# Performance work log

Hardware: AMD Instinct MI355X
Metric: run time of the kernel (lower is better)

The kernel has to match this reference:

```python
import jax, jax.numpy as jnp
import numpy as np
from jax import lax

ALPHA = 2.0  # ATan surrogate alpha (spikingjelly default)
V_TH = 1.0   # threshold; v_reset = 0.0 (hard reset)

@jax.custom_vjp
def spike_fn(x):
    return (x >= 0.0).astype(x.dtype)

def _spike_fwd(x):
    return spike_fn(x), x

def _spike_bwd(x, g):
    # ATan surrogate: alpha/2 / (1 + (pi/2*alpha*x)^2)
    sg = (ALPHA / 2.0) / (1.0 + (jnp.pi / 2.0 * ALPHA * x) ** 2)
    return (g * sg,)

spike_fn.defvjp(_spike_fwd, _spike_bwd)

def conv_bn(x_seq, w, gamma, beta, mean, var, eps=1e-5):
    # x_seq: [T,B,C,H,W]; conv+BN applied over flattened T*B (SeqToANNContainer)
    T, B, C, H, W = x_seq.shape
    y = lax.conv_general_dilated(
        x_seq.reshape(T * B, C, H, W), w,
        window_strides=(1, 1), padding='SAME',
        dimension_numbers=('NCHW', 'OIHW', 'NCHW'))
    inv = gamma / jnp.sqrt(var + eps)
    y = y * inv[None, :, None, None] + (beta - mean * inv)[None, :, None, None]
    Co = w.shape[0]
    return y.reshape(T, B, Co, H, W)

def plif(x_seq, w):
    # Parametric LIF: v <- v + (x - v) * sigmoid(w); hard reset to 0; detach_reset
    k = jax.nn.sigmoid(w)
    def step(v, x):
        v = v + (x - v) * k
        s = spike_fn(v - V_TH)
        v = v * (1.0 - lax.stop_gradient(s))
        return v, s
    _, s_seq = lax.scan(step, jnp.zeros_like(x_seq[0]), x_seq)
    return s_seq

def setup_inputs() -> dict:
    key = jax.random.key(0)
    ks = jax.random.split(key, 4)
    T, B, C, H, W = 4, 8, 128, 56, 56
    mid = 128
    x = (jax.random.uniform(ks[0], (T, B, C, H, W), jnp.float32) < 0.5).astype(jnp.float32)
    conv1_w = jax.random.normal(ks[1], (mid, C, 3, 3), jnp.float32) * (1.0 / np.sqrt(C * 9))
    conv2_w = jax.random.normal(ks[2], (C, mid, 3, 3), jnp.float32) * (1.0 / np.sqrt(mid * 9))
    return {
        'x': x,
        'conv1_w': conv1_w,
        'gamma1': jnp.ones((mid,), jnp.float32), 'beta1': jnp.zeros((mid,), jnp.float32),
        'mean1': jnp.zeros((mid,), jnp.float32), 'var1': jnp.ones((mid,), jnp.float32),
        'w1': jnp.float32(0.0),  # init_tau=2.0 -> w = -log(tau-1) = 0
        'conv2_w': conv2_w,
        'gamma2': jnp.ones((C,), jnp.float32), 'beta2': jnp.zeros((C,), jnp.float32),
        'mean2': jnp.zeros((C,), jnp.float32), 'var2': jnp.ones((C,), jnp.float32),
        'w2': jnp.float32(0.0),
    }

def reference(x, conv1_w, gamma1, beta1, mean1, var1, w1,
              conv2_w, gamma2, beta2, mean2, var2, w2):
    s1 = plif(conv_bn(x, conv1_w, gamma1, beta1, mean1, var1), w1)
    s2 = plif(conv_bn(s1, conv2_w, gamma2, beta2, mean2, var2), w2)
    out = s2 + x  # connect_f == 'ADD'
    return out
```

## Files before the change

kernel.cpp:

```cpp
#include <hip/hip_runtime.h>
#include <math.h>

#define T_ 4
#define B_ 8
#define C_ 128
#define H_ 56
#define W_ 56
#define NIMG (T_ * B_)
#define HW (H_ * W_)
#define NLOC ((size_t)B_ * C_ * HW)
#define NE ((size_t)T_ * NLOC)

typedef __attribute__((ext_vector_type(4))) int   int4v;
typedef __attribute__((ext_vector_type(4))) float float4v;

#define GLOAD_LDS16(gp, lp) \
    __builtin_amdgcn_global_load_lds((const __attribute__((address_space(1))) unsigned int*)(gp), \
                                     (__attribute__((address_space(3))) unsigned int*)(lp), 16, 0, 0)

__global__ __launch_bounds__(128) void scale_k(const float* __restrict__ w,
                                               float* __restrict__ sv) {
    __shared__ float red[128];
    int co = blockIdx.x, t = threadIdx.x;
    const float* p = w + (size_t)co * 1152 + t * 9;
    float m = 0.f;
#pragma unroll
    for (int j = 0; j < 9; ++j) m = fmaxf(m, fabsf(p[j]));
    red[t] = m; __syncthreads();
    for (int off = 64; off; off >>= 1) {
        if (t < off) red[t] = fmaxf(red[t], red[t + off]);
        __syncthreads();
    }
    if (t == 0) sv[co] = fmaxf(red[0], 1e-20f) / 127.f;
}

__global__ __launch_bounds__(256) void repack_k(const float* __restrict__ w,
                                                const float* __restrict__ sv,
                                                signed char* __restrict__ Bs) {
    int idx = blockIdx.x * 256 + threadIdx.x;
    if (idx >= 9 * 1024) return;
    int tap = idx >> 10;
    int rem = idx & 1023;
    int co = rem >> 3, cig = rem & 7;
    double s = (double)sv[co];
    union { signed char b[16]; int4v v; } q[3];
#pragma unroll
    for (int e = 0; e < 16; ++e) {
        int ci = cig * 16 + e;
        double v = (double)w[((size_t)co * 128 + ci) * 9 + tap];
        double q1 = rint(v / s);
        double r1 = v - s * q1;
        double q2 = rint(r1 * 128.0 / s);
        double r2 = r1 - s * q2 * 0.0078125;
        double q3 = rint(r2 * 16384.0 / s);
        q[0].b[e] = (signed char)(int)q1;
        q[1].b[e] = (signed char)(int)q2;
        q[2].b[e] = (signed char)(int)q3;
    }
    int Lb = co * 128 + ((cig ^ (co & 7)) << 4);
#pragma unroll
    for (int sp = 0; sp < 3; ++sp)
        *(int4v*)(Bs + (size_t)(tap * 3 + sp) * 16384 + Lb) = q[sp].v;
}

__global__ __launch_bounds__(256) void xpose_k(const float* __restrict__ x,
                                               signed char* __restrict__ Xt) {
    __shared__ float xs[128][57];
    int n = blockIdx.x / 56, h = blockIdx.x % 56;
    int tid = threadIdx.x;
    const float* xp = x + (size_t)n * 128 * HW + h * 56;
#pragma unroll
    for (int j = 0; j < 7; ++j) {
        int idx = tid + j * 256;
        int c = idx / 14, wq = idx - c * 14;
        float4 v = *(const float4*)(xp + (size_t)c * HW + wq * 4);
        xs[c][wq * 4 + 0] = v.x; xs[c][wq * 4 + 1] = v.y;
        xs[c][wq * 4 + 2] = v.z; xs[c][wq * 4 + 3] = v.w;
    }
    __syncthreads();
    signed char* Op = Xt + ((size_t)n * HW + h * 56) * 128;
#pragma unroll
    for (int j = 0; j < 2; ++j) {
        int idx = tid + j * 256;
        if (idx < 448) {
            int ww = idx >> 3, sl = idx & 7;
            int cg = sl ^ (ww & 7);
            union { signed char b[16]; int4v v; } u;
#pragma unroll
            for (int e = 0; e < 16; ++e)
                u.b[e] = (xs[cg * 16 + e][ww] >= 0.5f) ? 1 : 0;
            *(int4v*)(Op + ww * 128 + sl * 16) = u.v;
        }
    }
}

__global__ __launch_bounds__(512, 2) void conv_mfma_k(
        const signed char* __restrict__ Xt,
        const signed char* __restrict__ Bs,
        const float* __restrict__ sv,
        const float* __restrict__ gamma, const float* __restrict__ beta,
        const float* __restrict__ mean,  const float* __restrict__ var,
        float* __restrict__ Y) {
    __shared__ signed char aA[4 * 8192];
    __shared__ signed char bB[3 * 16384];

    const int tid = threadIdx.x;
    const int lane = tid & 63;
    const int wave = tid >> 6;
    const int fr = lane & 15, fq = lane >> 4;
    const int row_local = wave >> 2;
    const int q = wave & 3;
    const int img = blockIdx.x / 28;
    const int h0 = (blockIdx.x % 28) * 2;
    const int h = h0 + row_local;

#define STAGE3(tp) do {                                                           \
        const char* _src = (const char*)Bs + (size_t)(tp) * 49152 + tid * 16;     \
        char* _dst = (char*)bB + tid * 16;                                        \
        _Pragma("unroll")                                                         \
        for (int _c = 0; _c < 6; ++_c)                                            \
            GLOAD_LDS16(_src + _c * 8192, _dst + _c * 8192);                      \
    } while (0)

#define LOADA(tp) do {                                                            \
        int _dh = (tp) / 3, _dw = (tp) - ((tp) / 3) * 3;                          \
        int _hh = h + _dh - 1;                                                    \
        bool _hok = (unsigned)_hh < 56u;                                          \
        int _r4 = row_local + _dh;                                                \
        _Pragma("unroll")                                                         \
        for (int _m = 0; _m < 4; ++_m) {                                          \
            int _px = _m * 16 + fr + _dw - 1;                                     \
            bool _ok = _hok && ((unsigned)_px < 56u);                             \
            int _pxc = _ok ? _px : 0;                                             \
            const signed char* _base = aA + _r4 * 8192 + _pxc * 128;              \
            _Pragma("unroll")                                                     \
            for (int _ks = 0; _ks < 2; ++_ks) {                                   \
                int _sl = (_ks * 4 + fq) ^ (_pxc & 7);                            \
                int4v _v = *(const int4v*)(_base + _sl * 16);                     \
                a[_m][_ks] = _ok ? _v : zi;                                       \
            }                                                                     \
        }                                                                         \
    } while (0)

    const int tap0 = (int)((blockIdx.x * 4u) % 9u);

    {
        const signed char* XtN = Xt + (size_t)img * HW * 128;
#pragma unroll
        for (int i = 0; i < 4; ++i) {
            int hh = h0 - 1 + i;
            hh = hh < 0 ? 0 : (hh > 55 ? 55 : hh);
            const char* src = (const char*)(XtN + (size_t)hh * 7168);
            GLOAD_LDS16(src + tid * 16, (char*)aA + i * 8192 + tid * 16);
        }
        STAGE3(tap0);
        asm volatile("s_waitcnt vmcnt(0)" ::: "memory");
        __builtin_amdgcn_sched_barrier(0);
        __builtin_amdgcn_s_barrier();
    }

    const int4v zi = (int4v){0, 0, 0, 0};
    int4v acc[3][4][2];
#pragma unroll
    for (int sp = 0; sp < 3; ++sp)
#pragma unroll
        for (int m = 0; m < 4; ++m) {
            acc[sp][m][0] = zi; acc[sp][m][1] = zi;
        }
    int4v a[4][2];
    LOADA(tap0);

    const int cob = (q * 32 + fr) * 128;
    const int sl0 = (fq ^ (fr & 7)) << 4;
    const int sl1 = ((4 + fq) ^ (fr & 7)) << 4;

    for (int it = 0; it < 9; ++it) {
        int tap = tap0 + it; if (tap >= 9) tap -= 9;

        __builtin_amdgcn_s_setprio(1);
#pragma unroll
        for (int sp = 0; sp < 3; ++sp) {
            const signed char* bp = bB + sp * 16384;
            int4v b00 = *(const int4v*)(bp + cob + sl0);
            int4v b10 = *(const int4v*)(bp + cob + sl1);
            int4v b01 = *(const int4v*)(bp + cob + 2048 + sl0);
            int4v b11 = *(const int4v*)(bp + cob + 2048 + sl1);
#pragma unroll
            for (int m = 0; m < 4; ++m) {
                acc[sp][m][0] = __builtin_amdgcn_mfma_i32_16x16x64_i8(a[m][0], b00, acc[sp][m][0], 0, 0, 0);
                acc[sp][m][0] = __builtin_amdgcn_mfma_i32_16x16x64_i8(a[m][1], b10, acc[sp][m][0], 0, 0, 0);
                acc[sp][m][1] = __builtin_amdgcn_mfma_i32_16x16x64_i8(a[m][0], b01, acc[sp][m][1], 0, 0, 0);
                acc[sp][m][1] = __builtin_amdgcn_mfma_i32_16x16x64_i8(a[m][1], b11, acc[sp][m][1], 0, 0, 0);
            }
        }
        __builtin_amdgcn_s_setprio(0);
        __builtin_amdgcn_s_barrier();

        if (it < 8) {
            int ntap = tap + 1; if (ntap >= 9) ntap -= 9;
            STAGE3(ntap);
            LOADA(ntap);
            asm volatile("s_waitcnt vmcnt(0)" ::: "memory");
            __builtin_amdgcn_sched_barrier(0);
            __builtin_amdgcn_s_barrier();
        }
    }

    float* Yp = Y + ((size_t)img * HW + h * 56) * 128;
#pragma unroll
    for (int nf = 0; nf < 2; ++nf) {
        int co = q * 32 + nf * 16 + fr;
        float s = sv[co];
        float iv = gamma[co] / sqrtf(var[co] + 1e-5f);
        float mul = s * iv;
        float bs = beta[co] - mean[co] * iv;
#pragma unroll
        for (int m = 0; m < 4; ++m)
#pragma unroll
            for (int r = 0; r < 4; ++r) {
                int ww = m * 16 + fq * 4 + r;
                if (ww < 56) {
                    float val = (float)acc[0][m][nf][r]
                              + (float)acc[1][m][nf][r] * 0.0078125f
                              + (float)acc[2][m][nf][r] * 6.103515625e-05f;
                    Yp[(size_t)ww * 128 + co] = fmaf(val, mul, bs);
                }
            }
    }
#undef STAGE3
#undef LOADA
}

__global__ __launch_bounds__(256) void plif1_k(const float* __restrict__ Y,
                                               const float* __restrict__ wp,
                                               signed char* __restrict__ S) {
    int gid = blockIdx.x * 256 + threadIdx.x;
    int cg = gid & 7;
    int pix = gid >> 3;
    int w = (pix % HW) % 56;
    float k = 1.f / (1.f + expf(-wp[0]));
    float v[16];
#pragma unroll
    for (int e = 0; e < 16; ++e) v[e] = 0.f;
    size_t base = (size_t)pix * 128 + cg * 16;
    size_t obase = (size_t)pix * 128 + ((cg ^ (w & 7)) << 4);
#pragma unroll
    for (int t = 0; t < 4; ++t) {
        const float* yp = Y + (size_t)t * NLOC + base;
        union { signed char b[16]; int4v iv; } u;
#pragma unroll
        for (int e4 = 0; e4 < 4; ++e4) {
            float4 xv = *(const float4*)(yp + e4 * 4);
            float xe[4] = {xv.x, xv.y, xv.z, xv.w};
#pragma unroll
            for (int j = 0; j < 4; ++j) {
                int e = e4 * 4 + j;
                v[e] = v[e] + (xe[j] - v[e]) * k;
                bool sp = v[e] >= 1.f;
                u.b[e] = sp ? 1 : 0;
                v[e] = sp ? 0.f : v[e];
            }
        }
        *(int4v*)(S + (size_t)t * NLOC + obase) = u.iv;
    }
}

__global__ __launch_bounds__(256) void plif2_k(const float* __restrict__ Y2,
                                               const float* __restrict__ wp,
                                               const float* __restrict__ x,
                                               float* __restrict__ out) {
    __shared__ float xs[4 * 56 * 65];
    int bid = blockIdx.x;
    int half = bid & 1;
    int bh = bid >> 1;
    int b = bh / 56, h = bh % 56;
    int tid = threadIdx.x;
    float k = 1.f / (1.f + expf(-wp[0]));
#pragma unroll
    for (int j = 0; j < 14; ++j) {
        int idx = tid + j * 256;
        int t = idx / 896;
        int rem = idx - t * 896;
        int ww = rem >> 4, cq = rem & 15;
        float4 v = *(const float4*)(Y2 + ((size_t)(t * 8 + b) * HW + h * 56 + ww) * 128
                                       + half * 64 + cq * 4);
        float* dst = &xs[(t * 56 + ww) * 65 + cq * 4];
        dst[0] = v.x; dst[1] = v.y; dst[2] = v.z; dst[3] = v.w;
    }
    __syncthreads();
#pragma unroll
    for (int j = 0; j < 14; ++j) {
        int idx = tid + j * 256;
        int c = idx / 56, ww = idx - c * 56;
        float v = 0.f;
        size_t xo = ((size_t)b * 128 + half * 64 + c) * HW + h * 56 + ww;
#pragma unroll
        for (int t = 0; t < 4; ++t) {
            float yv = xs[(t * 56 + ww) * 65 + c];
            v = v + (yv - v) * k;
            bool sp = v >= 1.f;
            size_t o = xo + (size_t)t * NLOC;
            out[o] = (sp ? 1.f : 0.f) + x[o];
            v = sp ? 0.f : v;
        }
    }
}

extern "C" void kernel_launch(void* const* d_in, const int* in_sizes, int n_in,
                              void* d_out, int out_size, void* d_ws, size_t ws_size,
                              hipStream_t stream) {
    const float* x    = (const float*)d_in[0];
    const float* w1   = (const float*)d_in[1];
    const float* g1   = (const float*)d_in[2];
    const float* be1  = (const float*)d_in[3];
    const float* mu1  = (const float*)d_in[4];
    const float* va1  = (const float*)d_in[5];
    const float* tau1 = (const float*)d_in[6];
    const float* w2   = (const float*)d_in[7];
    const float* g2   = (const float*)d_in[8];
    const float* be2  = (const float*)d_in[9];
    const float* mu2  = (const float*)d_in[10];
    const float* va2  = (const float*)d_in[11];
    const float* tau2 = (const float*)d_in[12];
    float* out = (float*)d_out;

    char* ws = (char*)d_ws;
    signed char* bufA = (signed char*)ws;
    float* bufY = (float*)(ws + NE);
    float* sv1  = (float*)(ws + 5 * NE);
    float* sv2  = sv1 + 128;
    signed char* Bs1 = (signed char*)(ws + 5 * NE + 1024);
    signed char* Bs2 = Bs1 + 27 * 16384;

    scale_k<<<128, 128, 0, stream>>>(w1, sv1);
    scale_k<<<128, 128, 0, stream>>>(w2, sv2);
    repack_k<<<36, 256, 0, stream>>>(w1, sv1, Bs1);
    repack_k<<<36, 256, 0, stream>>>(w2, sv2, Bs2);
    xpose_k<<<NIMG * 56, 256, 0, stream>>>(x, bufA);

    conv_mfma_k<<<NIMG * 28, 512, 0, stream>>>(bufA, Bs1, sv1, g1, be1, mu1, va1, bufY);
    plif1_k<<<784, 256, 0, stream>>>(bufY, tau1, bufA);
    conv_mfma_k<<<NIMG * 28, 512, 0, stream>>>(bufA, Bs2, sv2, g2, be2, mu2, va2, bufY);
    plif2_k<<<B_ * 56 * 2, 256, 0, stream>>>(bufY, tau2, x, out);
}
```

Measured before the change: 197.8 us.

## Fuse conv with PLIF over time steps and double-buffer weight staging

Each conv block now loops over all four time steps of a batch image instead of handling one image. It keeps the PLIF membrane state in registers and applies BN, the spike update and either the int8 spike store or the residual add directly in the epilogue. This removes the fp32 intermediate write/read and the two separate PLIF kernels, and weight taps are double-buffered in LDS with partial vmcnt waits to overlap loads with MFMA. The trade-off is a grid cut to 224 large blocks with higher LDS use, which lowers occupancy and leaves some CUs idle.

```diff
diff --git a/kernel.cpp b/kernel.cpp
--- a/kernel.cpp
+++ b/kernel.cpp
@@ -12,7 +12,6 @@
 #define NE ((size_t)T_ * NLOC)
 
 typedef __attribute__((ext_vector_type(4))) int   int4v;
-typedef __attribute__((ext_vector_type(4))) float float4v;
 
 #define GLOAD_LDS16(gp, lp) \
     __builtin_amdgcn_global_load_lds((const __attribute__((address_space(1))) unsigned int*)(gp), \
@@ -94,15 +93,19 @@
     }
 }
 
-__global__ __launch_bounds__(512, 2) void conv_mfma_k(
-        const signed char* __restrict__ Xt,
+template<int MODE>
+__global__ __launch_bounds__(512) void convplif_k(
+        const signed char* __restrict__ Xin,
         const signed char* __restrict__ Bs,
         const float* __restrict__ sv,
         const float* __restrict__ gamma, const float* __restrict__ beta,
         const float* __restrict__ mean,  const float* __restrict__ var,
-        float* __restrict__ Y) {
+        const float* __restrict__ tau,
+        const float* __restrict__ xres,
+        void* __restrict__ outp) {
     __shared__ signed char aA[4 * 8192];
-    __shared__ signed char bB[3 * 16384];
+    __shared__ signed char bB[2][49152];
+    __shared__ signed char sS[2 * 8192];
 
     const int tid = threadIdx.x;
     const int lane = tid & 63;
@@ -110,13 +113,35 @@
     const int fr = lane & 15, fq = lane >> 4;
     const int row_local = wave >> 2;
     const int q = wave & 3;
-    const int img = blockIdx.x / 28;
+    const int bb = blockIdx.x / 28;
     const int h0 = (blockIdx.x % 28) * 2;
     const int h = h0 + row_local;
-
-#define STAGE3(tp) do {                                                           \
+    const int tap0 = (int)((blockIdx.x * 4u) % 9u);
+
+    const float kk = 1.f / (1.f + expf(-tau[0]));
+    float mulv[2], bsv[2];
+#pragma unroll
+    for (int nf = 0; nf < 2; ++nf) {
+        int co = q * 32 + nf * 16 + fr;
+        float iv = gamma[co] / sqrtf(var[co] + 1e-5f);
+        mulv[nf] = sv[co] * iv;
+        bsv[nf] = beta[co] - mean[co] * iv;
+    }
+
+#define STAGEA(tt) do {                                                           \
+        const signed char* _XtN = Xin + (size_t)((tt) * 8 + bb) * (HW * 128);     \
+        _Pragma("unroll")                                                         \
+        for (int _i = 0; _i < 4; ++_i) {                                          \
+            int _hh = h0 - 1 + _i;                                                \
+            _hh = _hh < 0 ? 0 : (_hh > 55 ? 55 : _hh);                            \
+            GLOAD_LDS16((const char*)(_XtN + (size_t)_hh * 7168) + tid * 16,      \
+                        (char*)aA + _i * 8192 + tid * 16);                        \
+        }                                                                         \
+    } while (0)
+
+#define STAGEB(tp, buf) do {                                                      \
         const char* _src = (const char*)Bs + (size_t)(tp) * 49152 + tid * 16;     \
-        char* _dst = (char*)bB + tid * 16;                                        \
+        char* _dst = (char*)&bB[(buf)][0] + tid * 16;                             \
         _Pragma("unroll")                                                         \
         for (int _c = 0; _c < 6; ++_c)                                            \
             GLOAD_LDS16(_src + _c * 8192, _dst + _c * 8192);                      \
@@ -142,31 +167,25 @@
         }                                                                         \
     } while (0)
 
-    const int tap0 = (int)((blockIdx.x * 4u) % 9u);
-
-    {
-        const signed char* XtN = Xt + (size_t)img * HW * 128;
-#pragma unroll
-        for (int i = 0; i < 4; ++i) {
-            int hh = h0 - 1 + i;
-            hh = hh < 0 ? 0 : (hh > 55 ? 55 : hh);
-            const char* src = (const char*)(XtN + (size_t)hh * 7168);
-            GLOAD_LDS16(src + tid * 16, (char*)aA + i * 8192 + tid * 16);
-        }
-        STAGE3(tap0);
-        asm volatile("s_waitcnt vmcnt(0)" ::: "memory");
-        __builtin_amdgcn_sched_barrier(0);
-        __builtin_amdgcn_s_barrier();
-    }
+    STAGEA(0);
+    STAGEB(tap0, 0);
+    asm volatile("s_waitcnt vmcnt(0)" ::: "memory");
+    __builtin_amdgcn_sched_barrier(0);
+    __builtin_amdgcn_s_barrier();
 
     const int4v zi = (int4v){0, 0, 0, 0};
     int4v acc[3][4][2];
 #pragma unroll
     for (int sp = 0; sp < 3; ++sp)
 #pragma unroll
-        for (int m = 0; m < 4; ++m) {
-            acc[sp][m][0] = zi; acc[sp][m][1] = zi;
-        }
+        for (int m = 0; m < 4; ++m) { acc[sp][m][0] = zi; acc[sp][m][1] = zi; }
+    float v[2][4][4];
+#pragma unroll
+    for (int nf = 0; nf < 2; ++nf)
+#pragma unroll
+        for (int m = 0; m < 4; ++m)
+#pragma unroll
+            for (int r = 0; r < 4; ++r) v[nf][m][r] = 0.f;
     int4v a[4][2];
     LOADA(tap0);
 
@@ -174,13 +193,25 @@
     const int sl0 = (fq ^ (fr & 7)) << 4;
     const int sl1 = ((4 + fq) ^ (fr & 7)) << 4;
 
-    for (int it = 0; it < 9; ++it) {
-        int tap = tap0 + it; if (tap >= 9) tap -= 9;
-
+    int tap = tap0, it = 0, t = 0;
+    for (int g = 0; g < 36; ++g) {
+        const int ntap = (tap + 1 == 9) ? 0 : tap + 1;
+        const bool tend = (it == 8);
+        if (tend && t < 3) STAGEA(t + 1);
+        if (g < 35) {
+            STAGEB(ntap, (g + 1) & 1);
+            asm volatile("s_waitcnt vmcnt(6)" ::: "memory");
+        } else {
+            asm volatile("s_waitcnt vmcnt(0)" ::: "memory");
+        }
+        __builtin_amdgcn_sched_barrier(0);
+        __builtin_amdgcn_s_barrier();
+
+        const signed char* bbase = &bB[g & 1][0];
         __builtin_amdgcn_s_setprio(1);
 #pragma unroll
         for (int sp = 0; sp < 3; ++sp) {
-            const signed char* bp = bB + sp * 16384;
+            const signed char* bp = bbase + sp * 16384;
             int4v b00 = *(const int4v*)(bp + cob + sl0);
             int4v b10 = *(const int4v*)(bp + cob + sl1);
             int4v b01 = *(const int4v*)(bp + cob + 2048 + sl0);
@@ -194,116 +225,90 @@
             }
         }
         __builtin_amdgcn_s_setprio(0);
+
+        if (g < 35) LOADA(ntap);
+        asm volatile("s_waitcnt lgkmcnt(0)" ::: "memory");
+        __builtin_amdgcn_sched_barrier(0);
         __builtin_amdgcn_s_barrier();
 
-        if (it < 8) {
-            int ntap = tap + 1; if (ntap >= 9) ntap -= 9;
-            STAGE3(ntap);
-            LOADA(ntap);
-            asm volatile("s_waitcnt vmcnt(0)" ::: "memory");
-            __builtin_amdgcn_sched_barrier(0);
-            __builtin_amdgcn_s_barrier();
-        }
-    }
-
-    float* Yp = Y + ((size_t)img * HW + h * 56) * 128;
-#pragma unroll
-    for (int nf = 0; nf < 2; ++nf) {
-        int co = q * 32 + nf * 16 + fr;
-        float s = sv[co];
-        float iv = gamma[co] / sqrtf(var[co] + 1e-5f);
-        float mul = s * iv;
-        float bs = beta[co] - mean[co] * iv;
-#pragma unroll
-        for (int m = 0; m < 4; ++m)
-#pragma unroll
-            for (int r = 0; r < 4; ++r) {
-                int ww = m * 16 + fq * 4 + r;
-                if (ww < 56) {
-                    float val = (float)acc[0][m][nf][r]
-                              + (float)acc[1][m][nf][r] * 0.0078125f
-                              + (float)acc[2][m][nf][r] * 6.103515625e-05f;
-                    Yp[(size_t)ww * 128 + co] = fmaf(val, mul, bs);
+        if (tend) {
+            if (MODE == 0) {
+                signed char* S1 = (signed char*)outp;
+#pragma unroll
+                for (int nf = 0; nf < 2; ++nf)
+#pragma unroll
+                    for (int m = 0; m < 4; ++m)
+#pragma unroll
+                        for (int r = 0; r < 4; ++r) {
+                            int px = m * 16 + fq * 4 + r;
+                            float val = (float)acc[0][m][nf][r]
+                                      + (float)acc[1][m][nf][r] * 0.0078125f
+                                      + (float)acc[2][m][nf][r] * 6.103515625e-05f;
+                            float y = fmaf(val, mulv[nf], bsv[nf]);
+                            float vv = v[nf][m][r];
+                            vv = vv + (y - vv) * kk;
+                            bool spk = vv >= 1.f;
+                            v[nf][m][r] = spk ? 0.f : vv;
+                            sS[row_local * 8192 + px * 128 + q * 32 + nf * 16 + fr] = spk ? 1 : 0;
+                        }
+                asm volatile("s_waitcnt lgkmcnt(0)" ::: "memory");
+                __builtin_amdgcn_s_barrier();
+                const size_t imgb = (size_t)(t * 8 + bb) * HW;
+#pragma unroll
+                for (int cc = 0; cc < 2; ++cc) {
+                    int chunk = tid + cc * 512;
+                    int row = chunk >> 9, rem = chunk & 511;
+                    int px = rem >> 3, cg = rem & 7;
+                    if (px < 56) {
+                        int4v v16 = *(const int4v*)(sS + row * 8192 + px * 128 + cg * 16);
+                        *(int4v*)(S1 + (imgb + (size_t)(h0 + row) * 56 + px) * 128
+                                     + ((cg ^ (px & 7)) << 4)) = v16;
+                    }
+                }
+            } else {
+                float* outw = (float*)outp;
+#pragma unroll
+                for (int nf = 0; nf < 2; ++nf) {
+                    const size_t cobase = ((size_t)(t * 8 + bb) * 128 + q * 32 + nf * 16 + fr) * HW
+                                        + (size_t)h * 56;
+#pragma unroll
+                    for (int m = 0; m < 4; ++m) {
+                        int px0 = m * 16 + fq * 4;
+                        float o4[4];
+#pragma unroll
+                        for (int r = 0; r < 4; ++r) {
+                            float val = (float)acc[0][m][nf][r]
+                                      + (float)acc[1][m][nf][r] * 0.0078125f
+                                      + (float)acc[2][m][nf][r] * 6.103515625e-05f;
+                            float y = fmaf(val, mulv[nf], bsv[nf]);
+                            float vv = v[nf][m][r];
+                            vv = vv + (y - vv) * kk;
+                            bool spk = vv >= 1.f;
+                            v[nf][m][r] = spk ? 0.f : vv;
+                            o4[r] = spk ? 1.f : 0.f;
+                        }
+                        if (px0 < 56) {
+                            float4 xv = *(const float4*)(xres + cobase + px0);
+                            float4 ov = make_float4(o4[0] + xv.x, o4[1] + xv.y,
+                                                    o4[2] + xv.z, o4[3] + xv.w);
+                            *(float4*)(outw + cobase + px0) = ov;
+                        }
+                    }
                 }
             }
-    }
-#undef STAGE3
+#pragma unroll
+            for (int sp = 0; sp < 3; ++sp)
+#pragma unroll
+                for (int m = 0; m < 4; ++m) { acc[sp][m][0] = zi; acc[sp][m][1] = zi; }
+            t++; it = 0;
+        } else {
+            it++;
+        }
+        tap = ntap;
+    }
+#undef STAGEA
+#undef STAGEB
 #undef LOADA
-}
-
-__global__ __launch_bounds__(256) void plif1_k(const float* __restrict__ Y,
-                                               const float* __restrict__ wp,
-                                               signed char* __restrict__ S) {
-    int gid = blockIdx.x * 256 + threadIdx.x;
-    int cg = gid & 7;
-    int pix = gid >> 3;
-    int w = (pix % HW) % 56;
-    float k = 1.f / (1.f + expf(-wp[0]));
-    float v[16];
-#pragma unroll
-    for (int e = 0; e < 16; ++e) v[e] = 0.f;
-    size_t base = (size_t)pix * 128 + cg * 16;
-    size_t obase = (size_t)pix * 128 + ((cg ^ (w & 7)) << 4);
-#pragma unroll
-    for (int t = 0; t < 4; ++t) {
-        const float* yp = Y + (size_t)t * NLOC + base;
-        union { signed char b[16]; int4v iv; } u;
-#pragma unroll
-        for (int e4 = 0; e4 < 4; ++e4) {
-            float4 xv = *(const float4*)(yp + e4 * 4);
-            float xe[4] = {xv.x, xv.y, xv.z, xv.w};
-#pragma unroll
-            for (int j = 0; j < 4; ++j) {
-                int e = e4 * 4 + j;
-                v[e] = v[e] + (xe[j] - v[e]) * k;
-                bool sp = v[e] >= 1.f;
-                u.b[e] = sp ? 1 : 0;
-                v[e] = sp ? 0.f : v[e];
-            }
-        }
-        *(int4v*)(S + (size_t)t * NLOC + obase) = u.iv;
-    }
-}
-
-__global__ __launch_bounds__(256) void plif2_k(const float* __restrict__ Y2,
-                                               const float* __restrict__ wp,
-                                               const float* __restrict__ x,
-                                               float* __restrict__ out) {
-    __shared__ float xs[4 * 56 * 65];
-    int bid = blockIdx.x;
-    int half = bid & 1;
-    int bh = bid >> 1;
-    int b = bh / 56, h = bh % 56;
-    int tid = threadIdx.x;
-    float k = 1.f / (1.f + expf(-wp[0]));
-#pragma unroll
-    for (int j = 0; j < 14; ++j) {
-        int idx = tid + j * 256;
-        int t = idx / 896;
-        int rem = idx - t * 896;
-        int ww = rem >> 4, cq = rem & 15;
-        float4 v = *(const float4*)(Y2 + ((size_t)(t * 8 + b) * HW + h * 56 + ww) * 128
-                                       + half * 64 + cq * 4);
-        float* dst = &xs[(t * 56 + ww) * 65 + cq * 4];
-        dst[0] = v.x; dst[1] = v.y; dst[2] = v.z; dst[3] = v.w;
-    }
-    __syncthreads();
-#pragma unroll
-    for (int j = 0; j < 14; ++j) {
-        int idx = tid + j * 256;
-        int c = idx / 56, ww = idx - c * 56;
-        float v = 0.f;
-        size_t xo = ((size_t)b * 128 + half * 64 + c) * HW + h * 56 + ww;
-#pragma unroll
-        for (int t = 0; t < 4; ++t) {
-            float yv = xs[(t * 56 + ww) * 65 + c];
-            v = v + (yv - v) * k;
-            bool sp = v >= 1.f;
-            size_t o = xo + (size_t)t * NLOC;
-            out[o] = (sp ? 1.f : 0.f) + x[o];
-            v = sp ? 0.f : v;
-        }
-    }
 }
 
 extern "C" void kernel_launch(void* const* d_in, const int* in_sizes, int n_in,
@@ -325,21 +330,21 @@
     float* out = (float*)d_out;
 
     char* ws = (char*)d_ws;
-    signed char* bufA = (signed char*)ws;
-    float* bufY = (float*)(ws + NE);
-    float* sv1  = (float*)(ws + 5 * NE);
+    signed char* Xt  = (signed char*)ws;
+    signed char* S1  = (signed char*)(ws + NE);
+    float* sv1  = (float*)(ws + 2 * NE);
     float* sv2  = sv1 + 128;
-    signed char* Bs1 = (signed char*)(ws + 5 * NE + 1024);
+    signed char* Bs1 = (signed char*)(ws + 2 * NE + 1024);
     signed char* Bs2 = Bs1 + 27 * 16384;
 
     scale_k<<<128, 128, 0, stream>>>(w1, sv1);
     scale_k<<<128, 128, 0, stream>>>(w2, sv2);
     repack_k<<<36, 256, 0, stream>>>(w1, sv1, Bs1);
     repack_k<<<36, 256, 0, stream>>>(w2, sv2, Bs2);
-    xpose_k<<<NIMG * 56, 256, 0, stream>>>(x, bufA);
-
-    conv_mfma_k<<<NIMG * 28, 512, 0, stream>>>(bufA, Bs1, sv1, g1, be1, mu1, va1, bufY);
-    plif1_k<<<784, 256, 0, stream>>>(bufY, tau1, bufA);
-    conv_mfma_k<<<NIMG * 28, 512, 0, stream>>>(bufA, Bs2, sv2, g2, be2, mu2, va2, bufY);
-    plif2_k<<<B_ * 56 * 2, 256, 0, stream>>>(bufY, tau2, x, out);
-}
+    xpose_k<<<NIMG * 56, 256, 0, stream>>>(x, Xt);
+
+    convplif_k<0><<<B_ * 28, 512, 0, stream>>>(Xt, Bs1, sv1, g1, be1, mu1, va1,
+                                               tau1, x, (void*)S1);
+    convplif_k<1><<<B_ * 28, 512, 0, stream>>>(S1, Bs2, sv2, g2, be2, mu2, va2,
+                                               tau2, x, (void*)out);
+}
```

Result: faster. 170.2 us (-14.0%).
